# Kernel optimization log

Hardware: AMD Instinct MI355X
Metric: run time of the kernel (lower is better)

Reference implementation:

```python
import jax, jax.numpy as jnp
import numpy as np

N = 100000       # nodes
E = 1600000      # undirected edges (one direction stored)
D = 64           # feature_dim


def _linear_params(key, fan_in, fan_out):
    kw, kb = jax.random.split(key)
    s = 1.0 / np.sqrt(fan_in)
    W = jax.random.uniform(kw, (fan_in, fan_out), jnp.float32, -s, s)
    b = jax.random.uniform(kb, (fan_out,), jnp.float32, -s, s)
    return W, b


def setup_inputs() -> dict:
    key = jax.random.key(0)
    ks = jax.random.split(key, 8)
    node_features = jax.random.normal(ks[0], (N, D), jnp.float32)
    node_operations = jax.random.normal(ks[1], (N, 4), jnp.float32)

    # Unique undirected edges, no self-loops -> torch's set() dedup of
    # {outgoing} U {incoming} neighbors equals counting each stored edge once
    # in both directions.
    rng = np.random.default_rng(0)
    src = rng.integers(0, N, size=4 * E)
    dst = rng.integers(0, N, size=4 * E)
    lo, hi = np.minimum(src, dst), np.maximum(src, dst)
    keep = lo != hi
    pairs = np.unique(np.stack([lo[keep], hi[keep]], axis=1), axis=0)
    assert pairs.shape[0] >= E
    perm = rng.permutation(pairs.shape[0])[:E]
    edge_index = jnp.asarray(pairs[perm].T, dtype=jnp.int32)  # [2, E]

    # node_generator: Linear(2D,128)-ReLU-Linear(128,64)-ReLU-Linear(64,D+3)
    W1, b1 = _linear_params(ks[2], 2 * D, 128)
    W2, b2 = _linear_params(ks[3], 128, 64)
    W3, b3 = _linear_params(ks[4], 64, D + 3)
    # insertion_predictor: Linear(D,32)-ReLU-Linear(32,1)-Sigmoid
    P1, pb1 = _linear_params(ks[5], D, 32)
    P2, pb2 = _linear_params(ks[6], 32, 1)

    return {
        'node_features': node_features,
        'node_operations': node_operations,
        'edge_index': edge_index,
        'W1': W1, 'b1': b1, 'W2': W2, 'b2': b2, 'W3': W3, 'b3': b3,
        'P1': P1, 'pb1': pb1, 'P2': P2, 'pb2': pb2,
    }


def reference(node_features, node_operations, edge_index,
              W1, b1, W2, b2, W3, b3, P1, pb1, P2, pb2):
    n = node_features.shape[0]
    src, dst = edge_index[0], edge_index[1]

    # candidate mask: softmax over op logits, class 0 = insert, threshold 0.5
    insert_probs = jax.nn.softmax(node_operations, axis=-1)[:, 0]
    ones = jnp.ones(src.shape[0], node_features.dtype)
    deg = (jax.ops.segment_sum(ones, src, num_segments=n)
           + jax.ops.segment_sum(ones, dst, num_segments=n))
    # torch loop skips candidates with no neighbors
    mask = (insert_probs > 0.5) & (deg > 0)
    maskf = mask.astype(node_features.dtype)

    # batched neighbor mean (undirected: both edge directions)
    nsum = (jax.ops.segment_sum(node_features[dst], src, num_segments=n)
            + jax.ops.segment_sum(node_features[src], dst, num_segments=n))
    nmean = nsum / jnp.maximum(deg, 1.0)[:, None]

    ctx = jnp.concatenate([node_features, nmean], axis=-1)  # [N, 2D]
    h = jax.nn.relu(ctx @ W1 + b1)
    h = jax.nn.relu(h @ W2 + b2)
    gen = h @ W3 + b3                         # [N, D+3]
    pos = gen[:, :3]                          # [N, 3]
    feats = gen[:, 3:]                        # [N, D]
    p = jax.nn.relu(feats @ P1 + pb1)
    prob = jax.nn.sigmoid(p @ P2 + pb2)       # [N, 1]

    # pack: [positions | features | probability], zeroed for non-candidates
    out = jnp.concatenate([pos, feats, prob], axis=-1) * maskf[:, None]
    return out
```

## Files before the change

kernel.cpp:

```cpp
#include <hip/hip_runtime.h>
#include <hip/hip_bf16.h>
#include <hip/hip_fp16.h>
#include <math.h>

typedef unsigned int u32;
typedef unsigned short u16;
typedef unsigned long long u64;

#define O_W1 0
#define O_b1 16384
#define O_W2 16512
#define O_b2 24704
#define O_W3 24768
#define O_b3 29056
#define O_P1 29123
#define O_pb1 31171
#define O_P2 31203
#define O_pb2 31235
#define W_TOTAL 31236

#define NPB 16
#define LDW 17

__device__ __forceinline__ float ldf(const void* p, long i, int dt) {
  if (dt == 1) { u32 v = ((const u16*)p)[i]; return __uint_as_float(v << 16); }
  if (dt == 2) { __half h = ((const __half*)p)[i]; return __half2float(h); }
  return ((const float*)p)[i];
}
__device__ __forceinline__ int ldei(const int* p, long i, int is64) {
  return is64 ? p[2 * i] : p[i];
}
__device__ __forceinline__ int bit_test(const u64* bits, int i) {
  return (int)((bits[i >> 6] >> (i & 63)) & 1ull);
}

extern "C" __global__ void kall_detect(const u32* __restrict__ feat,
                                       const u32* __restrict__ w1,
                                       const u32* __restrict__ ops,
                                       const u32* __restrict__ ei,
                                       int* __restrict__ hdr)
{
  int lane = threadIdx.x;
  int mode = blockIdx.x;
  if (mode == 3) {
    unsigned long long m0 = __ballot(ei[lane] == 0u);
    unsigned long long m1 = __ballot(ei[64 + lane] == 0u);
    if (lane == 0) hdr[2] = (__popcll(m0) + __popcll(m1) >= 32) ? 1 : 0;
    return;
  }
  const u32* p = (mode == 0) ? feat : (mode == 1) ? w1 : ops;
  int slot = (mode == 0) ? 0 : (mode == 1) ? 1 : 3;
  u32 w0 = p[lane];
  u32 w1v = p[64 + lane];
  u16 h[4] = { (u16)(w0 & 0xffff), (u16)(w0 >> 16),
               (u16)(w1v & 0xffff), (u16)(w1v >> 16) };
  int cb = 0;
#pragma unroll
  for (int t = 0; t < 4; ++t) {
    int e8 = (h[t] >> 7) & 0xff;
    cb += (e8 >= 110 && e8 <= 140) ? 1 : 0;
  }
  int ch = 0;
#pragma unroll
  for (int t = 0; t < 4; t += 2) {
    int e5 = (h[t] >> 10) & 0x1f;
    ch += (e5 >= 5 && e5 <= 18) ? 1 : 0;
  }
  __shared__ int sb[64], sh[64];
  sb[lane] = cb; sh[lane] = ch;
  __syncthreads();
  if (lane == 0) {
    int CB = 0, CH = 0;
    for (int t = 0; t < 64; ++t) { CB += sb[t]; CH += sh[t]; }
    int dt;
    if (CB >= 200) dt = 1;
    else if (CH >= 100) dt = 2;
    else dt = 0;
    hdr[slot] = dt;
  }
}

extern "C" __global__ void __launch_bounds__(256)
kw_conv(const void* __restrict__ W1, const void* __restrict__ b1,
        const void* __restrict__ W2, const void* __restrict__ b2,
        const void* __restrict__ W3, const void* __restrict__ b3,
        const void* __restrict__ P1, const void* __restrict__ pb1,
        const void* __restrict__ P2, const void* __restrict__ pb2,
        const int* __restrict__ hdr, float* __restrict__ wf)
{
  int i = blockIdx.x * 256 + threadIdx.x;
  if (i >= W_TOTAL) return;
  const void* s; int o;
  if      (i < O_b1)  { s = W1;  o = i; }
  else if (i < O_W2)  { s = b1;  o = i - O_b1; }
  else if (i < O_b2)  { s = W2;  o = i - O_W2; }
  else if (i < O_W3)  { s = b2;  o = i - O_b2; }
  else if (i < O_b3)  { s = W3;  o = i - O_W3; }
  else if (i < O_P1)  { s = b3;  o = i - O_b3; }
  else if (i < O_pb1) { s = P1;  o = i - O_P1; }
  else if (i < O_P2)  { s = pb1; o = i - O_pb1; }
  else if (i < O_pb2) { s = P2;  o = i - O_P2; }
  else                { s = pb2; o = i - O_pb2; }
  wf[i] = ldf(s, o, hdr[1]);
}

extern "C" __global__ void __launch_bounds__(256)
k2a_cand(const void* __restrict__ opsv, const int* __restrict__ hdr,
         u64* __restrict__ bits, int* __restrict__ cnt,
         int* __restrict__ fillcnt, int N)
{
  int i = blockIdx.x * 256 + threadIdx.x;
  if (i >= N) return;
  cnt[i] = 0;
  fillcnt[i] = 0;
  int dt = hdr[3];
  float x0 = ldf(opsv, (long)i * 4 + 0, dt);
  float x1 = ldf(opsv, (long)i * 4 + 1, dt);
  float x2 = ldf(opsv, (long)i * 4 + 2, dt);
  float x3 = ldf(opsv, (long)i * 4 + 3, dt);
  float m = fmaxf(fmaxf(x0, x1), fmaxf(x2, x3));
  double e0 = exp((double)(x0 - m));
  double e1 = exp((double)(x1 - m));
  double e2 = exp((double)(x2 - m));
  double e3 = exp((double)(x3 - m));
  double p0 = e0 / (((e0 + e1) + e2) + e3);
  u64 msk = __ballot(p0 > 0.5);
  if ((threadIdx.x & 63) == 0) bits[i >> 6] = msk;
}

extern "C" __global__ void __launch_bounds__(256)
k1a_cnt(const int* __restrict__ ei, const u64* __restrict__ bits,
        int* __restrict__ cnt, int E, const int* __restrict__ hdr)
{
  int e = blockIdx.x * 256 + threadIdx.x;
  if (e >= E) return;
  int is64 = hdr[2];
  int s = ldei(ei, e, is64);
  int d = ldei(ei, (long)E + e, is64);
  if (bit_test(bits, s)) atomicAdd(cnt + s, 1);
  if (bit_test(bits, d)) atomicAdd(cnt + d, 1);
}

extern "C" __global__ void __launch_bounds__(256)
k2b_alloc(const u64* __restrict__ bits, const int* __restrict__ cnt,
          int* __restrict__ hdr, int* __restrict__ nodeoff,
          int* __restrict__ nlist, int N)
{
  int i = blockIdx.x * 256 + threadIdx.x;
  if (i >= N) return;
  int c = (bit_test(bits, i) && cnt[i] > 0) ? cnt[i] : 0;
  if (c > 0) {
    int pos = atomicAdd(hdr + 4, 1);
    nlist[pos] = i;
    nodeoff[i] = atomicAdd(hdr + 5, c);
  } else {
    nodeoff[i] = -1;
  }
}

extern "C" __global__ void __launch_bounds__(256)
k1_fill(const int* __restrict__ ei, const u64* __restrict__ bits,
        const int* __restrict__ nodeoff,
        int* __restrict__ fillcnt, int* __restrict__ adj, int E,
        const int* __restrict__ hdr)
{
  int e = blockIdx.x * 256 + threadIdx.x;
  if (e >= E) return;
  int is64 = hdr[2];
  int s = ldei(ei, e, is64);
  int d = ldei(ei, (long)E + e, is64);
  if (bit_test(bits, s)) {
    int os = nodeoff[s];
    if (os >= 0) { int p = atomicAdd(fillcnt + s, 1); adj[os + p] = d; }
  }
  if (bit_test(bits, d)) {
    int od = nodeoff[d];
    if (od >= 0) { int p = atomicAdd(fillcnt + d, 1); adj[od + p] = s; }
  }
}

extern "C" __global__ void __launch_bounds__(256)
k3a_gather(const void* __restrict__ featv, const int* __restrict__ cnt,
           const int* __restrict__ nodeoff, const int* __restrict__ nlist,
           const int* __restrict__ adj, const int* __restrict__ hdr,
           float* __restrict__ out)
{
  const int lane = threadIdx.x & 63;
  const int q = __builtin_amdgcn_readfirstlane(threadIdx.x >> 6);
  const int dt = hdr[0];
  const int nmask = hdr[4];
  if (dt == 0) {
    const float4* f4 = (const float4*)featv;
    const int g = lane >> 4;
    const int fq = lane & 15;
    for (long b = (long)blockIdx.x * 4 + q; b < nmask; b += (long)gridDim.x * 4) {
      int node = nlist[b];
      int off = nodeoff[node];
      int dg = cnt[node];
      float4 acc = make_float4(0.f, 0.f, 0.f, 0.f);
      int j = g;
      for (; j + 4 < dg; j += 8) {
        int n0 = adj[off + j];
        int n1 = adj[off + j + 4];
        float4 v0 = f4[(long)n0 * 16 + fq];
        float4 v1 = f4[(long)n1 * 16 + fq];
        acc.x += v0.x + v1.x; acc.y += v0.y + v1.y;
        acc.z += v0.z + v1.z; acc.w += v0.w + v1.w;
      }
      if (j < dg) {
        int n0 = adj[off + j];
        float4 v0 = f4[(long)n0 * 16 + fq];
        acc.x += v0.x; acc.y += v0.y; acc.z += v0.z; acc.w += v0.w;
      }
      acc.x += __shfl_xor(acc.x, 16); acc.y += __shfl_xor(acc.y, 16);
      acc.z += __shfl_xor(acc.z, 16); acc.w += __shfl_xor(acc.w, 16);
      acc.x += __shfl_xor(acc.x, 32); acc.y += __shfl_xor(acc.y, 32);
      acc.z += __shfl_xor(acc.z, 32); acc.w += __shfl_xor(acc.w, 32);
      if (g == 0) {
        float inv = 1.f / (float)dg;
        float4 r = make_float4(acc.x * inv, acc.y * inv, acc.z * inv, acc.w * inv);
        *(float4*)(out + (long)node * 68 + fq * 4) = r;
      }
    }
  } else {
    for (long b = (long)blockIdx.x * 4 + q; b < nmask; b += (long)gridDim.x * 4) {
      int node = nlist[b];
      int off = nodeoff[node];
      int dg = cnt[node];
      float acc = 0.f;
      int j = 0;
      for (; j + 4 <= dg; j += 4) {
        int n0 = adj[off + j + 0];
        int n1 = adj[off + j + 1];
        int n2 = adj[off + j + 2];
        int n3 = adj[off + j + 3];
        float v0 = ldf(featv, (long)n0 * 64 + lane, dt);
        float v1 = ldf(featv, (long)n1 * 64 + lane, dt);
        float v2 = ldf(featv, (long)n2 * 64 + lane, dt);
        float v3 = ldf(featv, (long)n3 * 64 + lane, dt);
        acc += ((v0 + v1) + (v2 + v3));
      }
      for (; j < dg; ++j)
        acc += ldf(featv, (long)adj[off + j] * 64 + lane, dt);
      out[(long)node * 68 + lane] = acc / (float)dg;
    }
  }
}

extern "C" __global__ void __launch_bounds__(256)
k3b_mlp(const void* __restrict__ featv, const int* __restrict__ nlist,
        const float* __restrict__ wf, const int* __restrict__ hdr,
        float* __restrict__ out)
{
  __shared__ float A[128 * LDW];
  __shared__ float B[128 * LDW];
  __shared__ float WS[4096];
  __shared__ int sNode[NPB];
  const int tid = threadIdx.x;
  const int nmask = hdr[4];
  const int base = blockIdx.x * NPB;
  if (nmask == 0 || base >= nmask) return;
  const int dt = hdr[0];
  const int nl = tid & 15;
  const int jg = tid >> 4;

  if (tid < NPB) {
    int idx = base + tid;
    sNode[tid] = nlist[(idx < nmask) ? idx : (nmask - 1)];
  }
  __syncthreads();

#pragma unroll
  for (int i = 0; i < 8; ++i) {
    int g = i * 256 + tid;
    int f = g & 127;
    int n = g >> 7;
    int node = sNode[n];
    float v = (f < 64) ? ldf(featv, (long)node * 64 + f, dt)
                       : out[(long)node * 68 + (f - 64)];
    A[f * LDW + n] = v;
  }

  {
    const int j0 = jg * 8;
    float a0 = wf[O_b1 + j0 + 0], a1 = wf[O_b1 + j0 + 1];
    float a2 = wf[O_b1 + j0 + 2], a3 = wf[O_b1 + j0 + 3];
    float a4 = wf[O_b1 + j0 + 4], a5 = wf[O_b1 + j0 + 5];
    float a6 = wf[O_b1 + j0 + 6], a7 = wf[O_b1 + j0 + 7];
    for (int c = 0; c < 4; ++c) {
      __syncthreads();
      {
        const float4* s4 = (const float4*)(wf + O_W1 + c * 4096);
        float4* d4 = (float4*)WS;
#pragma unroll
        for (int i = 0; i < 4; ++i) d4[tid + 256 * i] = s4[tid + 256 * i];
      }
      __syncthreads();
#pragma unroll 4
      for (int k = 0; k < 32; ++k) {
        float x = A[(c * 32 + k) * LDW + nl];
        const float* w = WS + k * 128 + j0;
        float4 w0 = *(const float4*)(w);
        float4 w1 = *(const float4*)(w + 4);
        a0 = fmaf(x, w0.x, a0);
        a1 = fmaf(x, w0.y, a1);
        a2 = fmaf(x, w0.z, a2);
        a3 = fmaf(x, w0.w, a3);
        a4 = fmaf(x, w1.x, a4);
        a5 = fmaf(x, w1.y, a5);
        a6 = fmaf(x, w1.z, a6);
        a7 = fmaf(x, w1.w, a7);
      }
    }
    B[(j0 + 0) * LDW + nl] = fmaxf(a0, 0.f);
    B[(j0 + 1) * LDW + nl] = fmaxf(a1, 0.f);
    B[(j0 + 2) * LDW + nl] = fmaxf(a2, 0.f);
    B[(j0 + 3) * LDW + nl] = fmaxf(a3, 0.f);
    B[(j0 + 4) * LDW + nl] = fmaxf(a4, 0.f);
    B[(j0 + 5) * LDW + nl] = fmaxf(a5, 0.f);
    B[(j0 + 6) * LDW + nl] = fmaxf(a6, 0.f);
    B[(j0 + 7) * LDW + nl] = fmaxf(a7, 0.f);
  }

  {
    const int j0 = jg * 4;
    float a0 = wf[O_b2 + j0 + 0], a1 = wf[O_b2 + j0 + 1];
    float a2 = wf[O_b2 + j0 + 2], a3 = wf[O_b2 + j0 + 3];
    for (int c = 0; c < 2; ++c) {
      __syncthreads();
      {
        const float4* s4 = (const float4*)(wf + O_W2 + c * 4096);
        float4* d4 = (float4*)WS;
#pragma unroll
        for (int i = 0; i < 4; ++i) d4[tid + 256 * i] = s4[tid + 256 * i];
      }
      __syncthreads();
#pragma unroll 4
      for (int k = 0; k < 64; ++k) {
        float x = B[(c * 64 + k) * LDW + nl];
        float4 w = *(const float4*)(WS + k * 64 + j0);
        a0 = fmaf(x, w.x, a0);
        a1 = fmaf(x, w.y, a1);
        a2 = fmaf(x, w.z, a2);
        a3 = fmaf(x, w.w, a3);
      }
    }
    A[(j0 + 0) * LDW + nl] = fmaxf(a0, 0.f);
    A[(j0 + 1) * LDW + nl] = fmaxf(a1, 0.f);
    A[(j0 + 2) * LDW + nl] = fmaxf(a2, 0.f);
    A[(j0 + 3) * LDW + nl] = fmaxf(a3, 0.f);
  }

  {
    const int jq = jg;
    const bool has5 = (jq < 3);
    float a0 = 0.f, a1 = 0.f, a2 = 0.f, a3 = 0.f, a4 = 0.f;
    for (int c = 0; c < 2; ++c) {
      __syncthreads();
      {
        const float4* s4 = (const float4*)(wf + O_W3 + c * 2144);
        float4* d4 = (float4*)WS;
        for (int i = tid; i < 536; i += 256) d4[i] = s4[i];
      }
      __syncthreads();
#pragma unroll 4
      for (int k = 0; k < 32; ++k) {
        float x = A[(c * 32 + k) * LDW + nl];
        const float* w = WS + k * 67 + jq;
        float w4 = has5 ? w[64] : 0.f;
        a0 = fmaf(x, w[0],  a0);
        a1 = fmaf(x, w[16], a1);
        a2 = fmaf(x, w[32], a2);
        a3 = fmaf(x, w[48], a3);
        a4 = fmaf(x, w4,    a4);
      }
    }
    B[(jq +  0) * LDW + nl] = wf[O_b3 + jq]      + a0;
    B[(jq + 16) * LDW + nl] = wf[O_b3 + jq + 16] + a1;
    B[(jq + 32) * LDW + nl] = wf[O_b3 + jq + 32] + a2;
    B[(jq + 48) * LDW + nl] = wf[O_b3 + jq + 48] + a3;
    if (has5)
      B[(jq + 64) * LDW + nl] = wf[O_b3 + jq + 64] + a4;
  }

  {
    const int jq = jg;
    float a0 = wf[O_pb1 + jq], a1 = wf[O_pb1 + jq + 16];
    __syncthreads();
    for (int i = tid; i < 2048; i += 256) WS[i] = wf[O_P1 + i];
    __syncthreads();
#pragma unroll 4
    for (int k = 0; k < 64; ++k) {
      float x = B[(3 + k) * LDW + nl];
      a0 = fmaf(x, WS[k * 32 + jq],      a0);
      a1 = fmaf(x, WS[k * 32 + jq + 16], a1);
    }
    A[(jq +  0) * LDW + nl] = fmaxf(a0, 0.f);
    A[(jq + 16) * LDW + nl] = fmaxf(a1, 0.f);
  }
  __syncthreads();

  if (tid < 64) {
    const int part = tid >> 4;
    float p = 0.f;
#pragma unroll
    for (int kk = 0; kk < 8; ++kk) {
      int k = part * 8 + kk;
      p = fmaf(A[k * LDW + nl], wf[O_P2 + k], p);
    }
    p += __shfl_xor(p, 16);
    p += __shfl_xor(p, 32);
    if (part == 0) {
      float z = wf[O_pb2] + p;
      B[67 * LDW + nl] = 1.0f / (1.0f + expf(-z));
    }
  }
  __syncthreads();

  for (int g = tid; g < NPB * 68; g += 256) {
    int n = g / 68;
    int c = g - n * 68;
    if (base + n < nmask) {
      int node = sNode[n];
      out[(long)node * 68 + c] = B[c * LDW + n];
    }
  }
}

extern "C" void kernel_launch(void* const* d_in, const int* in_sizes, int n_in,
                              void* d_out, int out_size, void* d_ws, size_t ws_size,
                              hipStream_t stream) {
  int iF = 0, iO = 1, iE = 2;
  int iW1 = 3, ib1 = 4, iW2 = 5, ib2 = 6, iW3 = 7, ib3 = 8;
  int iP1 = 9, ipb1 = 10, iP2 = 11, ipb2 = 12;
  {
    int bigs[4]; int nb = 0;
    for (int i = 0; i < n_in && nb < 4; ++i)
      if (in_sizes[i] > 100000) bigs[nb++] = i;
    if (nb == 3) {
      int a = bigs[0], b = bigs[1], c = bigs[2];
      int mx = a, mn = a;
      if (in_sizes[b] > in_sizes[mx]) mx = b;
      if (in_sizes[c] > in_sizes[mx]) mx = c;
      if (in_sizes[b] < in_sizes[mn]) mn = b;
      if (in_sizes[c] < in_sizes[mn]) mn = c;
      iF = mx; iO = mn; iE = a + b + c - mx - mn;
      int t32[2]; int n32 = 0;
      int jW1=-1, jb1=-1, jW2=-1, jb2=-1, jW3=-1, jb3=-1, jP1=-1, jpb2=-1;
      for (int i = 0; i < n_in; ++i) {
        if (i == iF || i == iO || i == iE) continue;
        switch (in_sizes[i]) {
          case 16384: jW1 = i; break;
          case 128:   jb1 = i; break;
          case 8192:  jW2 = i; break;
          case 64:    jb2 = i; break;
          case 4288:  jW3 = i; break;
          case 67:    jb3 = i; break;
          case 2048:  jP1 = i; break;
          case 1:     jpb2 = i; break;
          case 32:    if (n32 < 2) t32[n32++] = i; break;
          default: break;
        }
      }
      if (jW1 >= 0 && jb1 >= 0 && jW2 >= 0 && jb2 >= 0 && jW3 >= 0 &&
          jb3 >= 0 && jP1 >= 0 && jpb2 >= 0 && n32 == 2) {
        iW1 = jW1; ib1 = jb1; iW2 = jW2; ib2 = jb2; iW3 = jW3; ib3 = jb3;
        iP1 = jP1; ipb2 = jpb2;
        if (t32[1] == t32[0] + 1) { ipb1 = t32[0]; iP2 = t32[1]; }
        else                      { iP2 = t32[0]; ipb1 = t32[1]; }
      }
    }
  }
  int N = (out_size % 68 == 0) ? (out_size / 68) : (in_sizes[iF] / 64);
  const int E = in_sizes[iE] / 2;
  const void* feat = d_in[iF];
  const void* ops  = d_in[iO];
  const int* ei    = (const int*)d_in[iE];

  char* ws = (char*)d_ws;
  int* hdr = (int*)ws;
  size_t off = 256;
  float* wf = (float*)(ws + off);
  off += ((size_t)W_TOTAL * 4 + 255) & ~(size_t)255;
  u64* bits = (u64*)(ws + off);
  off += (((size_t)(N + 63) / 64) * 8 + 255) & ~(size_t)255;
  int* cnt = (int*)(ws + off);
  off += ((size_t)N * 4 + 255) & ~(size_t)255;
  int* nodeoff = (int*)(ws + off);
  off += ((size_t)N * 4 + 255) & ~(size_t)255;
  int* fillcnt = (int*)(ws + off);
  off += ((size_t)N * 4 + 255) & ~(size_t)255;
  int* nlist = (int*)(ws + off);
  off += ((size_t)N * 4 + 255) & ~(size_t)255;
  int* adj = (int*)(ws + off);

  hipMemsetAsync(hdr, 0, 256, stream);
  hipMemsetAsync(d_out, 0, (size_t)out_size * 4, stream);

  kall_detect<<<4, 64, 0, stream>>>((const u32*)feat, (const u32*)d_in[iW1],
                                    (const u32*)ops, (const u32*)ei, hdr);

  kw_conv<<<(W_TOTAL + 255) / 256, 256, 0, stream>>>(
      d_in[iW1], d_in[ib1], d_in[iW2], d_in[ib2], d_in[iW3], d_in[ib3],
      d_in[iP1], d_in[ipb1], d_in[iP2], d_in[ipb2], hdr, wf);
  k2a_cand<<<(N + 255) / 256, 256, 0, stream>>>(ops, hdr, bits, cnt, fillcnt, N);
  k1a_cnt<<<(E + 255) / 256, 256, 0, stream>>>(ei, bits, cnt, E, hdr);
  k2b_alloc<<<(N + 255) / 256, 256, 0, stream>>>(bits, cnt, hdr, nodeoff, nlist, N);
  k1_fill<<<(E + 255) / 256, 256, 0, stream>>>(ei, bits, nodeoff, fillcnt, adj, E, hdr);
  k3a_gather<<<2048, 256, 0, stream>>>(feat, cnt, nodeoff, nlist, adj, hdr,
                                       (float*)d_out);
  k3b_mlp<<<(N + NPB - 1) / NPB, 256, 0, stream>>>(feat, nlist, wf, hdr,
                                                   (float*)d_out);
}
```

Measured before the change: 240.5 us.

## Fuse neighbor-mean gather into MLP kernel, writing means straight to shared memory

Merges the separate gather kernel into the MLP kernel. Each block gathers neighbor features for its 16 candidate nodes, with 4 nodes per wavefront, and writes the means directly into the shared A tile. This removes one kernel launch and the global write and read-back of the mean vectors through the output buffer. In exchange, gather latency now sits inside the MLP block and can be uneven across blocks, and the old persistent grid-stride scheduling is gone.

```diff
diff --git a/kernel.cpp b/kernel.cpp
--- a/kernel.cpp
+++ b/kernel.cpp
@@ -180,23 +180,55 @@
 }
 
 extern "C" __global__ void __launch_bounds__(256)
-k3a_gather(const void* __restrict__ featv, const int* __restrict__ cnt,
-           const int* __restrict__ nodeoff, const int* __restrict__ nlist,
-           const int* __restrict__ adj, const int* __restrict__ hdr,
-           float* __restrict__ out)
-{
-  const int lane = threadIdx.x & 63;
-  const int q = __builtin_amdgcn_readfirstlane(threadIdx.x >> 6);
+k3b_mlp(const void* __restrict__ featv, const int* __restrict__ nlist,
+        const int* __restrict__ cnt, const int* __restrict__ nodeoff,
+        const int* __restrict__ adj,
+        const float* __restrict__ wf, const int* __restrict__ hdr,
+        float* __restrict__ out)
+{
+  __shared__ float A[128 * LDW];
+  __shared__ float B[128 * LDW];
+  __shared__ float WS[4096];
+  __shared__ int sNode[NPB];
+  __shared__ int sDeg[NPB];
+  __shared__ int sOff[NPB];
+  const int tid = threadIdx.x;
+  const int nmask = hdr[4];
+  const int base = blockIdx.x * NPB;
+  if (nmask == 0 || base >= nmask) return;
   const int dt = hdr[0];
-  const int nmask = hdr[4];
+  const int nl = tid & 15;
+  const int jg = tid >> 4;
+  const int lane = tid & 63;
+  const int q = __builtin_amdgcn_readfirstlane(tid >> 6);
+
+  if (tid < NPB) {
+    int idx = base + tid;
+    int node = nlist[(idx < nmask) ? idx : (nmask - 1)];
+    sNode[tid] = node;
+    sDeg[tid] = cnt[node];
+    sOff[tid] = nodeoff[node];
+  }
+  __syncthreads();
+
+#pragma unroll
+  for (int i = 0; i < 4; ++i) {
+    int g = i * 256 + tid;
+    int f = g & 63;
+    int n = g >> 6;
+    int node = sNode[n];
+    A[f * LDW + n] = ldf(featv, (long)node * 64 + f, dt);
+  }
+
   if (dt == 0) {
     const float4* f4 = (const float4*)featv;
     const int g = lane >> 4;
     const int fq = lane & 15;
-    for (long b = (long)blockIdx.x * 4 + q; b < nmask; b += (long)gridDim.x * 4) {
-      int node = nlist[b];
-      int off = nodeoff[node];
-      int dg = cnt[node];
+#pragma unroll
+    for (int t = 0; t < 4; ++t) {
+      const int n = q * 4 + t;
+      const int off = sOff[n];
+      const int dg = sDeg[n];
       float4 acc = make_float4(0.f, 0.f, 0.f, 0.f);
       int j = g;
       for (; j + 4 < dg; j += 8) {
@@ -218,15 +250,18 @@
       acc.z += __shfl_xor(acc.z, 32); acc.w += __shfl_xor(acc.w, 32);
       if (g == 0) {
         float inv = 1.f / (float)dg;
-        float4 r = make_float4(acc.x * inv, acc.y * inv, acc.z * inv, acc.w * inv);
-        *(float4*)(out + (long)node * 68 + fq * 4) = r;
+        A[(64 + fq * 4 + 0) * LDW + n] = acc.x * inv;
+        A[(64 + fq * 4 + 1) * LDW + n] = acc.y * inv;
+        A[(64 + fq * 4 + 2) * LDW + n] = acc.z * inv;
+        A[(64 + fq * 4 + 3) * LDW + n] = acc.w * inv;
       }
     }
   } else {
-    for (long b = (long)blockIdx.x * 4 + q; b < nmask; b += (long)gridDim.x * 4) {
-      int node = nlist[b];
-      int off = nodeoff[node];
-      int dg = cnt[node];
+#pragma unroll
+    for (int t = 0; t < 4; ++t) {
+      const int n = q * 4 + t;
+      const int off = sOff[n];
+      const int dg = sDeg[n];
       float acc = 0.f;
       int j = 0;
       for (; j + 4 <= dg; j += 4) {
@@ -242,43 +277,8 @@
       }
       for (; j < dg; ++j)
         acc += ldf(featv, (long)adj[off + j] * 64 + lane, dt);
-      out[(long)node * 68 + lane] = acc / (float)dg;
-    }
-  }
-}
-
-extern "C" __global__ void __launch_bounds__(256)
-k3b_mlp(const void* __restrict__ featv, const int* __restrict__ nlist,
-        const float* __restrict__ wf, const int* __restrict__ hdr,
-        float* __restrict__ out)
-{
-  __shared__ float A[128 * LDW];
-  __shared__ float B[128 * LDW];
-  __shared__ float WS[4096];
-  __shared__ int sNode[NPB];
-  const int tid = threadIdx.x;
-  const int nmask = hdr[4];
-  const int base = blockIdx.x * NPB;
-  if (nmask == 0 || base >= nmask) return;
-  const int dt = hdr[0];
-  const int nl = tid & 15;
-  const int jg = tid >> 4;
-
-  if (tid < NPB) {
-    int idx = base + tid;
-    sNode[tid] = nlist[(idx < nmask) ? idx : (nmask - 1)];
-  }
-  __syncthreads();
-
-#pragma unroll
-  for (int i = 0; i < 8; ++i) {
-    int g = i * 256 + tid;
-    int f = g & 127;
-    int n = g >> 7;
-    int node = sNode[n];
-    float v = (f < 64) ? ldf(featv, (long)node * 64 + f, dt)
-                       : out[(long)node * 68 + (f - 64)];
-    A[f * LDW + n] = v;
+      A[(64 + lane) * LDW + n] = acc / (float)dg;
+    }
   }
 
   {
@@ -507,8 +507,7 @@
   k1a_cnt<<<(E + 255) / 256, 256, 0, stream>>>(ei, bits, cnt, E, hdr);
   k2b_alloc<<<(N + 255) / 256, 256, 0, stream>>>(bits, cnt, hdr, nodeoff, nlist, N);
   k1_fill<<<(E + 255) / 256, 256, 0, stream>>>(ei, bits, nodeoff, fillcnt, adj, E, hdr);
-  k3a_gather<<<2048, 256, 0, stream>>>(feat, cnt, nodeoff, nlist, adj, hdr,
-                                       (float*)d_out);
-  k3b_mlp<<<(N + NPB - 1) / NPB, 256, 0, stream>>>(feat, nlist, wf, hdr,
+  k3b_mlp<<<(N + NPB - 1) / NPB, 256, 0, stream>>>(feat, nlist, cnt, nodeoff,
+                                                   adj, wf, hdr,
                                                    (float*)d_out);
 }
```

After: 241.2 us. No clear change (+0.3%).
